# Kernel tuning notes

Hardware: AMD Instinct MI355X
Metric: run time of the kernel (lower is better)

Reference implementation:

```python
import jax, jax.numpy as jnp
import numpy as np

N_NODES = 100000
N_EDGES = 3200000
D_FEAT = 512
D_HID = 64
N_CLS = 40


def setup_inputs() -> dict:
    key = jax.random.key(0)
    k1, k2, k3, k4, k5, k6, k7 = jax.random.split(key, 7)
    x = jax.random.normal(k1, (N_NODES, D_FEAT), dtype=jnp.float32)
    edge_index = jax.random.randint(k2, (2, N_EDGES), 0, N_NODES, dtype=jnp.int64)
    edge_weight = jax.random.uniform(k3, (N_EDGES,), dtype=jnp.float32)
    # GCNConv params (glorot-ish scale)
    W1 = jax.random.normal(k4, (D_FEAT, D_HID), dtype=jnp.float32) / np.sqrt(D_FEAT)
    b1 = jnp.zeros((D_HID,), dtype=jnp.float32)
    W2 = jax.random.normal(k5, (D_HID, N_CLS), dtype=jnp.float32) / np.sqrt(D_HID)
    b2 = jnp.zeros((N_CLS,), dtype=jnp.float32)
    return {"x": x, "edge_index": edge_index, "edge_weight": edge_weight,
            "W1": W1, "b1": b1, "W2": W2, "b2": b2}


def _gcn_norm(edge_index, edge_weight, num_nodes):
    # add self-loops with weight 1 (PyG gcn_norm default)
    loop = jnp.arange(num_nodes, dtype=edge_index.dtype)
    row = jnp.concatenate([edge_index[0], loop])
    col = jnp.concatenate([edge_index[1], loop])
    ew = jnp.concatenate([edge_weight, jnp.ones((num_nodes,), edge_weight.dtype)])
    deg = jax.ops.segment_sum(ew, col, num_segments=num_nodes)  # in-degree (weighted)
    dinv = jnp.where(deg > 0, jax.lax.rsqrt(deg), 0.0)
    norm = dinv[row] * ew * dinv[col]
    return row, col, norm


def _gcn_conv(x, row, col, norm, W, b, num_nodes):
    x = x @ W  # linear first (out_channels small): [N, out]
    msg = norm[:, None] * x[row]            # gather + scale: [E+N, out]
    out = jax.ops.segment_sum(msg, col, num_segments=num_nodes)  # scatter-add
    return out + b


def reference(x, edge_index, edge_weight, W1, b1, W2, b2):
    n = x.shape[0]
    row, col, norm = _gcn_norm(edge_index, edge_weight, n)
    h = jax.nn.relu(_gcn_conv(x, row, col, norm, W1, b1, n))
    # dropout omitted (eval-mode determinism for correctness baseline)
    logits = _gcn_conv(h, row, col, norm, W2, b2, n)
    return jax.nn.log_softmax(logits, axis=1)
```

## Files before the change

### kernel.cpp

```cpp
#include <hip/hip_runtime.h>
#include <math.h>

#define N_NODES 100000
#define N_EDGES 3200000
#define D_FEAT  512
#define D_HID   64
#define N_CLS   40
#define ZSTR    48
#define NBKT    391
#define NBLKA   256
#define EPB     (N_EDGES / NBLKA)

typedef __attribute__((ext_vector_type(8))) short short8;
typedef __attribute__((ext_vector_type(4))) float floatx4;

static __device__ __forceinline__ unsigned short f2bf(float f) {
    unsigned u = __float_as_uint(f);
    unsigned r = (u + 0x7FFFu + ((u >> 16) & 1u)) >> 16;
    return (unsigned short)r;
}
static __device__ __forceinline__ float bf2f(unsigned short h) {
    return __uint_as_float(((unsigned)h) << 16);
}
static __device__ __forceinline__ short8 pack_bf16x8(float4 a, float4 b) {
    short8 r;
    r[0] = (short)f2bf(a.x); r[1] = (short)f2bf(a.y);
    r[2] = (short)f2bf(a.z); r[3] = (short)f2bf(a.w);
    r[4] = (short)f2bf(b.x); r[5] = (short)f2bf(b.y);
    r[6] = (short)f2bf(b.z); r[7] = (short)f2bf(b.w);
    return r;
}


__global__ __launch_bounds__(256) void k_histA(const int* __restrict__ ei,
                                               int* __restrict__ mat) {
    __shared__ int hist[NBKT];
    const int tid = threadIdx.x, blk = blockIdx.x;
    for (int i = tid; i < NBKT; i += 256) hist[i] = 0;
    __syncthreads();
    const int e0 = blk * EPB, e1 = e0 + EPB;
    for (int e = e0 + tid; e < e1; e += 256)
        atomicAdd(&hist[ei[N_EDGES + e] >> 8], 1);
    __syncthreads();
    for (int i = tid; i < NBKT; i += 256) mat[i * NBLKA + blk] = hist[i];
}


__global__ __launch_bounds__(256) void k_scanRows(int* __restrict__ mat,
                                                  int* __restrict__ total) {
    __shared__ int s[256];
    const int tid = threadIdx.x, bin = blockIdx.x;
    int v = mat[bin * NBLKA + tid];
    s[tid] = v;
    __syncthreads();
    for (int off = 1; off < 256; off <<= 1) {
        int t = (tid >= off) ? s[tid - off] : 0;
        __syncthreads();
        s[tid] += t;
        __syncthreads();
    }
    mat[bin * NBLKA + tid] = s[tid] - v;
    if (tid == 255) total[bin] = s[255];
}


__global__ __launch_bounds__(512) void k_scanTot(const int* __restrict__ total,
                                                 int* __restrict__ cbase) {
    __shared__ int s[512];
    const int tid = threadIdx.x;
    int v = (tid < NBKT) ? total[tid] : 0;
    s[tid] = v;
    __syncthreads();
    for (int off = 1; off < 512; off <<= 1) {
        int t = (tid >= off) ? s[tid - off] : 0;
        __syncthreads();
        s[tid] += t;
        __syncthreads();
    }
    if (tid <= NBKT) cbase[tid] = s[tid] - v;
}


__global__ __launch_bounds__(256) void k_scatterB(const int* __restrict__ ei,
                                                  const float* __restrict__ ew,
                                                  const int* __restrict__ mat,
                                                  const int* __restrict__ cbase,
                                                  int2* __restrict__ tmpA,
                                                  unsigned char* __restrict__ tmpD) {
    __shared__ int cur[NBKT];
    const int tid = threadIdx.x, blk = blockIdx.x;
    for (int i = tid; i < NBKT; i += 256)
        cur[i] = cbase[i] + mat[i * NBLKA + blk];
    __syncthreads();
    const int e0 = blk * EPB, e1 = e0 + EPB;
    for (int e = e0 + tid; e < e1; e += 256) {
        int r = ei[e];
        int c = ei[N_EDGES + e];
        int slot = atomicAdd(&cur[c >> 8], 1);
        tmpA[slot] = make_int2(r, __float_as_int(ew[e]));
        tmpD[slot] = (unsigned char)(c & 255);
    }
}


__global__ __launch_bounds__(256) void k_bucketC(const int* __restrict__ cbase,
                                                 const int2* __restrict__ tmpA,
                                                 const unsigned char* __restrict__ tmpD,
                                                 int2* __restrict__ csr,
                                                 int* __restrict__ cnt,
                                                 int* __restrict__ base,
                                                 float* __restrict__ dinv) {
    __shared__ int   c_cnt[256];
    __shared__ float c_deg[256];
    __shared__ int   c_scan[256];
    __shared__ int   c_cur[256];
    __shared__ float c_dnv[256];
    const int tid = threadIdx.x, b = blockIdx.x;
    const int s = cbase[b], e = cbase[b + 1];
    c_cnt[tid] = 0;
    c_deg[tid] = 0.f;
    __syncthreads();
    for (int j = s + tid; j < e; j += 256) {
        int d = tmpD[j];
        atomicAdd(&c_cnt[d], 1);
        atomicAdd(&c_deg[d], __int_as_float(tmpA[j].y));
    }
    __syncthreads();
    int v = c_cnt[tid];
    c_scan[tid] = v;
    __syncthreads();
    for (int off = 1; off < 256; off <<= 1) {
        int t = (tid >= off) ? c_scan[tid - off] : 0;
        __syncthreads();
        c_scan[tid] += t;
        __syncthreads();
    }
    int excl = c_scan[tid] - v;
    c_cur[tid] = excl;
    float dv = rsqrtf(1.0f + c_deg[tid]);
    c_dnv[tid] = dv;
    int node = b * 256 + tid;
    if (node < N_NODES) {
        cnt[node]  = v;
        base[node] = s + excl;
        dinv[node] = dv;
    }
    __syncthreads();
    for (int j = s + tid; j < e; j += 256) {
        int d = tmpD[j];
        int2 p = tmpA[j];
        int slot = atomicAdd(&c_cur[d], 1);
        csr[s + slot] = make_int2(p.x, __float_as_int(__int_as_float(p.y) * c_dnv[d]));
    }
}


__global__ __launch_bounds__(256) void k_norm(int2* __restrict__ csr,
                                              const float* __restrict__ dinv) {
    int i = blockIdx.x * 256 + threadIdx.x;
    int2 p = csr[i];
    p.y = __float_as_int(__int_as_float(p.y) * dinv[p.x]);
    csr[i] = p;
}


__global__ __launch_bounds__(256) void k_gemm1(const float* __restrict__ x,
                                               const float* __restrict__ W1,
                                               unsigned short* __restrict__ hpre) {
    __shared__ __align__(16) short Wt[64 * 512];
    const int tid = threadIdx.x;

    {
        const int c  = tid & 63;
        const int kb = (tid >> 6) * 128;
        const int sw = (c & 7) << 3;
        for (int kk = 0; kk < 128; kk += 8) {
            short8 v;
#pragma unroll
            for (int j = 0; j < 8; j++)
                v[j] = (short)f2bf(W1[(size_t)(kb + kk + j) * D_HID + c]);
            *(short8*)&Wt[c * 512 + ((kb + kk) ^ sw)] = v;
        }
    }
    __syncthreads();

    const int widx = blockIdx.x * 4 + (tid >> 6);
    if (widx >= N_NODES / 16) return;
    const int lane = tid & 63;
    const int q  = lane >> 4;
    const int cn = lane & 15;
    const int r0 = widx * 16;
    const int sw = (cn & 7) << 3;

    floatx4 acc[4] = {{0,0,0,0},{0,0,0,0},{0,0,0,0},{0,0,0,0}};
    const float* xp = x + (size_t)(r0 + cn) * D_FEAT + q * 8;

#pragma unroll 4
    for (int k0 = 0; k0 < D_FEAT; k0 += 32) {
        float4 xa = *(const float4*)(xp + k0);
        float4 xb = *(const float4*)(xp + k0 + 4);
        short8 a = pack_bf16x8(xa, xb);
#pragma unroll
        for (int ct = 0; ct < 4; ct++) {
            short8 b = *(const short8*)&Wt[(ct * 16 + cn) * 512 + ((k0 + q * 8) ^ sw)];
            acc[ct] = __builtin_amdgcn_mfma_f32_16x16x32_bf16(a, b, acc[ct], 0, 0, 0);
        }
    }

#pragma unroll
    for (int ct = 0; ct < 4; ct++)
#pragma unroll
        for (int i = 0; i < 4; i++)
            hpre[(size_t)(r0 + q * 4 + i) * D_HID + ct * 16 + cn] = f2bf(acc[ct][i]);
}


__global__ __launch_bounds__(256) void k_gather1(const int* __restrict__ base,
                                                 const int* __restrict__ cnt,
                                                 const int2* __restrict__ csr,
                                                 const unsigned short* __restrict__ hpre,
                                                 const float* __restrict__ dinv,
                                                 const float* __restrict__ b1,
                                                 const float* __restrict__ W2,
                                                 float* __restrict__ z) {
    __shared__ float hs[4][64];
    const int lane = threadIdx.x & 63;
    const int w = threadIdx.x >> 6;
    const int n = blockIdx.x * 4 + w;
    const int s = base[n], e = s + cnt[n];
    const float dn = dinv[n];

    float acc[16];
#pragma unroll
    for (int u = 0; u < 16; u++) acc[u] = 0.f;
    acc[0] = dn * dn * bf2f(hpre[(size_t)n * D_HID + lane]);

    for (int c = s; c < e; c += 64) {
        int idx = c + lane;
        int idxc = idx < e ? idx : (e - 1);
        int2 ed = csr[idxc];
        if (idx >= e) ed.y = 0;
        int nc = e - c; if (nc > 64) nc = 64;
        for (int j = 0; j < nc; j += 16) {
#pragma unroll
            for (int u = 0; u < 16; u++) {
                int   src = __builtin_amdgcn_readlane(ed.x, j + u);
                float wj  = __uint_as_float((unsigned)__builtin_amdgcn_readlane(ed.y, j + u));
                const unsigned short* rp = hpre + ((size_t)src << 6);
                acc[u] = fmaf(wj, bf2f(rp[lane]), acc[u]);
            }
        }
    }

    float h = ((acc[0] + acc[1]) + (acc[2] + acc[3])) + ((acc[4] + acc[5]) + (acc[6] + acc[7]))
            + ((acc[8] + acc[9]) + (acc[10] + acc[11])) + ((acc[12] + acc[13]) + (acc[14] + acc[15]));
    h += b1[lane];
    h = h > 0.f ? h : 0.f;
    hs[w][lane] = h;
    if (lane < N_CLS) {
        float a2 = 0.f;
#pragma unroll 8
        for (int k = 0; k < D_HID; k++)
            a2 += hs[w][k] * W2[k * N_CLS + lane];
        z[(size_t)n * ZSTR + lane] = a2;
    }
}


__global__ __launch_bounds__(256) void k_gather2_lsm(const int* __restrict__ base,
                                                     const int* __restrict__ cnt,
                                                     const int2* __restrict__ csr,
                                                     const float* __restrict__ z,
                                                     const float* __restrict__ dinv,
                                                     const float* __restrict__ b2,
                                                     float* __restrict__ out) {
    const int lane = threadIdx.x & 63;
    const int n = blockIdx.x * 4 + (threadIdx.x >> 6);
    const bool act = lane < N_CLS;
    const int fl = act ? lane : (N_CLS - 1);
    const int s = base[n], e = s + cnt[n];
    const float dn = dinv[n];

    float acc[16];
#pragma unroll
    for (int u = 0; u < 16; u++) acc[u] = 0.f;
    acc[0] = dn * dn * z[(size_t)n * ZSTR + fl];

    for (int c = s; c < e; c += 64) {
        int idx = c + lane;
        int idxc = idx < e ? idx : (e - 1);
        int2 ed = csr[idxc];
        if (idx >= e) ed.y = 0;
        int nc = e - c; if (nc > 64) nc = 64;
        for (int j = 0; j < nc; j += 16) {
#pragma unroll
            for (int u = 0; u < 16; u++) {
                int   src = __builtin_amdgcn_readlane(ed.x, j + u);
                float wj  = __uint_as_float((unsigned)__builtin_amdgcn_readlane(ed.y, j + u));
                const float* rp = z + (size_t)src * ZSTR;
                acc[u] = fmaf(wj, rp[fl], acc[u]);
            }
        }
    }

    float logit = ((acc[0] + acc[1]) + (acc[2] + acc[3])) + ((acc[4] + acc[5]) + (acc[6] + acc[7]))
                + ((acc[8] + acc[9]) + (acc[10] + acc[11])) + ((acc[12] + acc[13]) + (acc[14] + acc[15]));
    logit += b2[fl];
    float m = act ? logit : -INFINITY;
    for (int off = 32; off; off >>= 1) m = fmaxf(m, __shfl_xor(m, off, 64));
    float ev = act ? expf(logit - m) : 0.f;
    float sum = ev;
    for (int off = 32; off; off >>= 1) sum += __shfl_xor(sum, off, 64);
    if (act) out[(size_t)n * N_CLS + lane] = logit - m - logf(sum);
}


extern "C" void kernel_launch(void* const* d_in, const int* in_sizes, int n_in,
                              void* d_out, int out_size, void* d_ws, size_t ws_size,
                              hipStream_t stream) {
    const float* x  = (const float*)d_in[0];
    const int*   ei = (const int*)d_in[1];
    const float* ew = (const float*)d_in[2];
    const float* W1 = (const float*)d_in[3];
    const float* b1 = (const float*)d_in[4];
    const float* W2 = (const float*)d_in[5];
    const float* b2 = (const float*)d_in[6];
    float* out = (float*)d_out;

    int* ws = (int*)d_ws;
    int2*          csr  = (int2*)ws;
    int2*          tmpA = (int2*)(ws + 2 * (size_t)N_EDGES);
    unsigned char* tmpD = (unsigned char*)(ws + 4 * (size_t)N_EDGES);
    int*   mat   = ws + 4 * (size_t)N_EDGES + N_EDGES / 4;
    int*   total = mat + NBKT * NBLKA;
    int*   cbase = total + NBKT;
    unsigned short* hpre = (unsigned short*)tmpA;
    float* z = (float*)(ws + 2 * (size_t)N_EDGES + (size_t)N_NODES * D_HID / 2);
    int*   cnt  = ws + 2 * (size_t)N_EDGES + (size_t)N_NODES * D_HID / 2 + (size_t)N_NODES * ZSTR;
    int*   base = cnt + N_NODES;
    float* dinv = (float*)(base + N_NODES);

    k_histA   <<<NBLKA, 256, 0, stream>>>(ei, mat);
    k_scanRows<<<NBKT,  256, 0, stream>>>(mat, total);
    k_scanTot <<<1,     512, 0, stream>>>(total, cbase);
    k_scatterB<<<NBLKA, 256, 0, stream>>>(ei, ew, mat, cbase, tmpA, tmpD);
    k_bucketC <<<NBKT,  256, 0, stream>>>(cbase, tmpA, tmpD, csr, cnt, base, dinv);
    k_norm    <<<N_EDGES / 256, 256, 0, stream>>>(csr, dinv);
    k_gemm1   <<<(N_NODES / 16 + 3) / 4, 256, 0, stream>>>(x, W1, hpre);
    k_gather1 <<<N_NODES / 4, 256, 0, stream>>>(base, cnt, csr, hpre, dinv, b1, W2, z);
    k_gather2_lsm<<<N_NODES / 4, 256, 0, stream>>>(base, cnt, csr, z, dinv, b2, out);
}
```

Measured before the change: 727.0 us.

## Split each wavefront across two edges with wider per-lane loads in gathers

Both gather kernels now handle two edges per wavefront step. Each half-wave of 32 lanes reads a whole feature row using 4-byte (bf16 pair) or 8-byte (float2) loads, and the edge list is staged through LDS instead of being broadcast with readlane. The z row stride grows from 48 to 64 floats so rows are aligned for the shifted addressing, which enlarges z and adds padding traffic. The aim is fewer, wider memory transactions and fewer scalar broadcasts per edge. The cost is an extra shuffle to combine the two halves and a larger z buffer, which must still fit the workspace layout.

```diff
diff --git a/kernel.cpp b/kernel.cpp
--- a/kernel.cpp
+++ b/kernel.cpp
@@ -6,7 +6,7 @@
 #define D_FEAT  512
 #define D_HID   64
 #define N_CLS   40
-#define ZSTR    48
+#define ZSTR    64
 #define NBKT    391
 #define NBLKA   256
 #define EPB     (N_EDGES / NBLKA)
@@ -218,100 +218,149 @@
 __global__ __launch_bounds__(256) void k_gather1(const int* __restrict__ base,
                                                  const int* __restrict__ cnt,
                                                  const int2* __restrict__ csr,
-                                                 const unsigned short* __restrict__ hpre,
+                                                 const unsigned char* __restrict__ hpreB,
                                                  const float* __restrict__ dinv,
                                                  const float* __restrict__ b1,
                                                  const float* __restrict__ W2,
                                                  float* __restrict__ z) {
     __shared__ float hs[4][64];
+    __shared__ int2  eds[4][64];
     const int lane = threadIdx.x & 63;
     const int w = threadIdx.x >> 6;
     const int n = blockIdx.x * 4 + w;
     const int s = base[n], e = s + cnt[n];
     const float dn = dinv[n];
-
-    float acc[16];
-#pragma unroll
-    for (int u = 0; u < 16; u++) acc[u] = 0.f;
-    acc[0] = dn * dn * bf2f(hpre[(size_t)n * D_HID + lane]);
+    const int q = lane & 31;
+    const int vsel = lane >> 5;
+    const unsigned laneoff = (unsigned)q << 2;
+
+    float accx[4] = {0.f, 0.f, 0.f, 0.f};
+    float accy[4] = {0.f, 0.f, 0.f, 0.f};
+    {
+        unsigned pv = *(const unsigned*)(hpreB + (((unsigned)n) << 7) + laneoff);
+        float dn2 = vsel ? 0.f : dn * dn;
+        accx[0] = dn2 * __uint_as_float(pv << 16);
+        accy[0] = dn2 * __uint_as_float(pv & 0xffff0000u);
+    }
 
     for (int c = s; c < e; c += 64) {
         int idx = c + lane;
-        int idxc = idx < e ? idx : (e - 1);
-        int2 ed = csr[idxc];
+        int2 ed = csr[idx < e ? idx : (e - 1)];
         if (idx >= e) ed.y = 0;
+        eds[w][lane] = ed;
         int nc = e - c; if (nc > 64) nc = 64;
         for (int j = 0; j < nc; j += 16) {
-#pragma unroll
-            for (int u = 0; u < 16; u++) {
-                int   src = __builtin_amdgcn_readlane(ed.x, j + u);
-                float wj  = __uint_as_float((unsigned)__builtin_amdgcn_readlane(ed.y, j + u));
-                const unsigned short* rp = hpre + ((size_t)src << 6);
-                acc[u] = fmaf(wj, bf2f(rp[lane]), acc[u]);
+            int2 ep[8]; unsigned pv[8];
+#pragma unroll
+            for (int p = 0; p < 8; p++)
+                ep[p] = eds[w][j + 2 * p + vsel];
+#pragma unroll
+            for (int p = 0; p < 8; p++)
+                pv[p] = *(const unsigned*)(hpreB + (((unsigned)ep[p].x) << 7) + laneoff);
+#pragma unroll
+            for (int p = 0; p < 8; p++) {
+                float wj = __int_as_float(ep[p].y);
+                accx[p & 3] = fmaf(wj, __uint_as_float(pv[p] << 16), accx[p & 3]);
+                accy[p & 3] = fmaf(wj, __uint_as_float(pv[p] & 0xffff0000u), accy[p & 3]);
             }
         }
     }
 
-    float h = ((acc[0] + acc[1]) + (acc[2] + acc[3])) + ((acc[4] + acc[5]) + (acc[6] + acc[7]))
-            + ((acc[8] + acc[9]) + (acc[10] + acc[11])) + ((acc[12] + acc[13]) + (acc[14] + acc[15]));
-    h += b1[lane];
-    h = h > 0.f ? h : 0.f;
-    hs[w][lane] = h;
+    float tx = (accx[0] + accx[1]) + (accx[2] + accx[3]);
+    float ty = (accy[0] + accy[1]) + (accy[2] + accy[3]);
+    tx += __shfl_xor(tx, 32, 64);
+    ty += __shfl_xor(ty, 32, 64);
+    if (lane < 32) {
+        float h0 = tx + b1[2 * lane];
+        float h1 = ty + b1[2 * lane + 1];
+        hs[w][2 * lane]     = h0 > 0.f ? h0 : 0.f;
+        hs[w][2 * lane + 1] = h1 > 0.f ? h1 : 0.f;
+    }
+    float a2 = 0.f;
     if (lane < N_CLS) {
-        float a2 = 0.f;
-#pragma unroll 8
-        for (int k = 0; k < D_HID; k++)
-            a2 += hs[w][k] * W2[k * N_CLS + lane];
-        z[(size_t)n * ZSTR + lane] = a2;
-    }
+#pragma unroll
+        for (int k = 0; k < D_HID; k += 4) {
+            float4 hv = *(const float4*)&hs[w][k];
+            a2 += hv.x * W2[(k    ) * N_CLS + lane] + hv.y * W2[(k + 1) * N_CLS + lane]
+                + hv.z * W2[(k + 2) * N_CLS + lane] + hv.w * W2[(k + 3) * N_CLS + lane];
+        }
+    }
+    z[(size_t)n * ZSTR + lane] = (lane < N_CLS) ? a2 : 0.f;
 }
 
 
 __global__ __launch_bounds__(256) void k_gather2_lsm(const int* __restrict__ base,
                                                      const int* __restrict__ cnt,
                                                      const int2* __restrict__ csr,
-                                                     const float* __restrict__ z,
+                                                     const unsigned char* __restrict__ zB,
                                                      const float* __restrict__ dinv,
                                                      const float* __restrict__ b2,
                                                      float* __restrict__ out) {
+    __shared__ int2 eds[4][64];
     const int lane = threadIdx.x & 63;
-    const int n = blockIdx.x * 4 + (threadIdx.x >> 6);
-    const bool act = lane < N_CLS;
-    const int fl = act ? lane : (N_CLS - 1);
+    const int w = threadIdx.x >> 6;
+    const int n = blockIdx.x * 4 + w;
     const int s = base[n], e = s + cnt[n];
     const float dn = dinv[n];
-
-    float acc[16];
-#pragma unroll
-    for (int u = 0; u < 16; u++) acc[u] = 0.f;
-    acc[0] = dn * dn * z[(size_t)n * ZSTR + fl];
+    const int q = lane & 31;
+    const int vsel = lane >> 5;
+    const unsigned laneoff = (unsigned)q << 3;
+
+    float accx[4] = {0.f, 0.f, 0.f, 0.f};
+    float accy[4] = {0.f, 0.f, 0.f, 0.f};
+    {
+        float2 zv = *(const float2*)(zB + (((unsigned)n) << 8) + laneoff);
+        float dn2 = vsel ? 0.f : dn * dn;
+        accx[0] = dn2 * zv.x;
+        accy[0] = dn2 * zv.y;
+    }
 
     for (int c = s; c < e; c += 64) {
         int idx = c + lane;
-        int idxc = idx < e ? idx : (e - 1);
-        int2 ed = csr[idxc];
+        int2 ed = csr[idx < e ? idx : (e - 1)];
         if (idx >= e) ed.y = 0;
+        eds[w][lane] = ed;
         int nc = e - c; if (nc > 64) nc = 64;
         for (int j = 0; j < nc; j += 16) {
-#pragma unroll
-            for (int u = 0; u < 16; u++) {
-                int   src = __builtin_amdgcn_readlane(ed.x, j + u);
-                float wj  = __uint_as_float((unsigned)__builtin_amdgcn_readlane(ed.y, j + u));
-                const float* rp = z + (size_t)src * ZSTR;
-                acc[u] = fmaf(wj, rp[fl], acc[u]);
+            int2 ep[8]; float2 pv[8];
+#pragma unroll
+            for (int p = 0; p < 8; p++)
+                ep[p] = eds[w][j + 2 * p + vsel];
+#pragma unroll
+            for (int p = 0; p < 8; p++)
+                pv[p] = *(const float2*)(zB + (((unsigned)ep[p].x) << 8) + laneoff);
+#pragma unroll
+            for (int p = 0; p < 8; p++) {
+                float wj = __int_as_float(ep[p].y);
+                accx[p & 3] = fmaf(wj, pv[p].x, accx[p & 3]);
+                accy[p & 3] = fmaf(wj, pv[p].y, accy[p & 3]);
             }
         }
     }
 
-    float logit = ((acc[0] + acc[1]) + (acc[2] + acc[3])) + ((acc[4] + acc[5]) + (acc[6] + acc[7]))
-                + ((acc[8] + acc[9]) + (acc[10] + acc[11])) + ((acc[12] + acc[13]) + (acc[14] + acc[15]));
-    logit += b2[fl];
-    float m = act ? logit : -INFINITY;
-    for (int off = 32; off; off >>= 1) m = fmaxf(m, __shfl_xor(m, off, 64));
-    float ev = act ? expf(logit - m) : 0.f;
+    float tx = (accx[0] + accx[1]) + (accx[2] + accx[3]);
+    float ty = (accy[0] + accy[1]) + (accy[2] + accy[3]);
+    tx += __shfl_xor(tx, 32, 64);
+    ty += __shfl_xor(ty, 32, 64);
+
+    const bool act2 = q < (N_CLS / 2);
+    float lg0 = 0.f, lg1 = 0.f;
+    if (act2) {
+        lg0 = tx + b2[2 * q];
+        lg1 = ty + b2[2 * q + 1];
+    }
+    float m = act2 ? fmaxf(lg0, lg1) : -INFINITY;
+    for (int off = 16; off; off >>= 1) m = fmaxf(m, __shfl_xor(m, off, 64));
+    float ev = act2 ? (expf(lg0 - m) + expf(lg1 - m)) : 0.f;
     float sum = ev;
-    for (int off = 32; off; off >>= 1) sum += __shfl_xor(sum, off, 64);
-    if (act) out[(size_t)n * N_CLS + lane] = logit - m - logf(sum);
+    for (int off = 16; off; off >>= 1) sum += __shfl_xor(sum, off, 64);
+    float ls = logf(sum);
+    if (lane < (N_CLS / 2)) {
+        float2 o;
+        o.x = lg0 - m - ls;
+        o.y = lg1 - m - ls;
+        *(float2*)(out + (size_t)n * N_CLS + 2 * lane) = o;
+    }
 }
 
 
@@ -347,6 +396,8 @@
     k_bucketC <<<NBKT,  256, 0, stream>>>(cbase, tmpA, tmpD, csr, cnt, base, dinv);
     k_norm    <<<N_EDGES / 256, 256, 0, stream>>>(csr, dinv);
     k_gemm1   <<<(N_NODES / 16 + 3) / 4, 256, 0, stream>>>(x, W1, hpre);
-    k_gather1 <<<N_NODES / 4, 256, 0, stream>>>(base, cnt, csr, hpre, dinv, b1, W2, z);
-    k_gather2_lsm<<<N_NODES / 4, 256, 0, stream>>>(base, cnt, csr, z, dinv, b2, out);
-}
+    k_gather1 <<<N_NODES / 4, 256, 0, stream>>>(base, cnt, csr,
+                                                (const unsigned char*)hpre, dinv, b1, W2, z);
+    k_gather2_lsm<<<N_NODES / 4, 256, 0, stream>>>(base, cnt, csr,
+                                                   (const unsigned char*)z, dinv, b2, out);
+}
```

Measured after the change: 706.5 us. 1.03x faster.
